# Kernel optimization log

Hardware: AMD Instinct MI355X
Metric: run time of the kernel (lower is better)

## Reference

```python
import jax, jax.numpy as jnp
import numpy as np

B, T, V, F, NH = 2, 1, 4, 128, 9
EMB_ZOOM = 5
N = 12 * 4 ** EMB_ZOOM        # 12288 grid cells at emb_zoom
NUP = 4 * N                   # 49152 cells at zoom emb_zoom+1
NVARS = 8


def setup_inputs() -> dict:
    key = jax.random.key(0)
    ks = jax.random.split(key, 8)
    embeddings = jax.random.normal(ks[0], (NVARS, N, F), dtype=jnp.float32)
    x5 = jax.random.normal(ks[1], (B, T, V, N, F), dtype=jnp.float32)
    x6 = jax.random.normal(ks[2], (B, T, V, NUP, F), dtype=jnp.float32)
    W5 = jax.random.normal(ks[3], (F, 2 * F), dtype=jnp.float32) / np.sqrt(F)
    b5 = jnp.zeros((2 * F,), dtype=jnp.float32)
    W6 = jax.random.normal(ks[4], (NH * F, 8 * F), dtype=jnp.float32) / np.sqrt(NH * F)
    b6 = jnp.zeros((8 * F,), dtype=jnp.float32)
    var_idx = jax.random.randint(ks[5], (B, T, V), 0, NVARS)
    adjc = jax.random.randint(ks[6], (N, NH), 0, N)
    adjc = adjc.at[:, 0].set(jnp.arange(N))  # column 0 is the self index
    return {"embeddings": embeddings, "x5": x5, "x6": x6,
            "W5": W5, "b5": b5, "W6": W6, "b6": b6,
            "var_idx": var_idx, "adjc": adjc}


def reference(embeddings, x5, x6, W5, b5, W6, b6, var_idx, adjc):
    # per-variable embedding selection: (B,T,V,N,F)
    embs = embeddings[var_idx]

    # --- zoom == emb_zoom: gather self index, Linear(F -> 2F), FiLM ---
    e5 = jnp.take(embs, adjc[:, 0], axis=-2)          # (B,T,V,N,F)
    h5 = e5 @ W5 + b5                                  # (B,T,V,N,2F)
    scale5, shift5 = jnp.split(h5, 2, axis=-1)
    y5 = x5 * scale5 + shift5

    # --- zoom == emb_zoom+1: gather full neighborhood, Linear(9F -> 4*2F), FiLM ---
    e6 = jnp.take(embs, adjc.reshape(-1), axis=-2)     # (B,T,V,N*NH,F)
    e6 = e6.reshape(B, T, V, N, NH * F)
    h6 = (e6 @ W6 + b6).reshape(B, T, V, NUP, 2 * F)   # 4 children per coarse cell
    scale6, shift6 = jnp.split(h6, 2, axis=-1)
    y6 = x6 * scale6 + shift6

    return (y5, y6)
```

## Files before the change

kernel.cpp:

```cpp
#include <hip/hip_runtime.h>
#include <stdint.h>

#define F_     128
#define N_     12288
#define NH_    9
#define NSLOT_ 8
#define NVARS_ 8
#define NUP_   (4*N_)
#define K6_    (NH_*F_)

typedef __attribute__((ext_vector_type(8))) short bf16x8;
typedef __attribute__((ext_vector_type(4))) float f32x4;

typedef const __attribute__((address_space(1))) unsigned char* gp1_t;
typedef __attribute__((address_space(3))) unsigned char* lp3_t;

__device__ __forceinline__ void load16(const void* g, void* l) {
  __builtin_amdgcn_global_load_lds((gp1_t)g, (lp3_t)l, 16, 0, 0);
}

__device__ __forceinline__ unsigned short f2bf(float f) {
  union { float f; unsigned int u; } x; x.f = f;
  unsigned int u = x.u;
  unsigned int r = u + 0x7FFFu + ((u >> 16) & 1u);
  return (unsigned short)(r >> 16);
}

__global__ void k_conv_emb(const float4* __restrict__ src, ushort4* __restrict__ dst, int n4) {
  int i = blockIdx.x * blockDim.x + threadIdx.x;
  if (i >= n4) return;
  float4 v = src[i];
  ushort4 o;
  o.x = f2bf(v.x); o.y = f2bf(v.y); o.z = f2bf(v.z); o.w = f2bf(v.w);
  dst[i] = o;
}

__global__ void k_transpose_bf(const float* __restrict__ src, unsigned short* __restrict__ dst,
                               int rows, int cols) {
  int i = blockIdx.x * blockDim.x + threadIdx.x;
  if (i >= rows * cols) return;
  int j = i / rows, k = i % rows;
  dst[i] = f2bf(src[k * cols + j]);
}

__global__ __launch_bounds__(256) void k_h5(
    const unsigned short* __restrict__ embB,
    const unsigned short* __restrict__ W5T,
    const float* __restrict__ b5,
    const float* __restrict__ x5,
    const int* __restrict__ var_idx,
    const int* __restrict__ adjc,
    float* __restrict__ y5)
{
  const int slot = blockIdx.y;
  const int var = var_idx[slot];
  for (int j = 0; j < NSLOT_; ++j) {
    if (j >= slot) break;
    if (var_idx[j] == var) return;
  }
  unsigned int fmask = 0;
  for (int j = slot; j < NSLOT_; ++j)
    if (var_idx[j] == var) fmask |= 1u << j;

  __shared__ __align__(1024) unsigned char smem[8192 + 32768 + 64*4];
  unsigned char* Asm = smem;
  unsigned char* Bsm = smem + 8192;
  int* ald = (int*)(smem + 8192 + 32768);

  const int tid = threadIdx.x;
  const int l = tid & 63, w = tid >> 6;
  const int wr = w >> 1, wc = w & 1;
  const int li8 = l >> 3, pc = l & 7, l15 = l & 15, l16 = l >> 4;

  const int nt = blockIdx.x;
  const int n0 = nt * 64;

  if (tid < 64) ald[tid] = adjc[(n0 + tid) * NH_];
  __syncthreads();

  const f32x4 fz = {0.f, 0.f, 0.f, 0.f};
  f32x4 accS[2][4], accH[2][4];
#pragma unroll
  for (int mf = 0; mf < 2; ++mf)
#pragma unroll
    for (int nf = 0; nf < 4; ++nf) { accS[mf][nf] = fz; accH[mf][nf] = fz; }

  const size_t embVarOff = (size_t)var * ((size_t)N_ * F_);

  for (int step = 0; step < 2; ++step) {
    const int k0 = step << 6;
#pragma unroll
    for (int q2 = 0; q2 < 2; ++q2) {
      const int q = w * 2 + q2;
      const int r = q * 8 + li8;
      const int lc = pc ^ (r & 7);
      const unsigned short* g = embB + embVarOff + (size_t)ald[r] * F_ + k0 + lc * 8;
      load16(g, Asm + q * 1024);
    }
#pragma unroll
    for (int q2 = 0; q2 < 8; ++q2) {
      const int q = w * 8 + q2;
      const int j = q * 8 + li8;
      const int lc = pc ^ (j & 7);
      const unsigned short* g = W5T + (size_t)j * F_ + k0 + lc * 8;
      load16(g, Bsm + q * 1024);
    }
    __syncthreads();

#pragma unroll
    for (int kf = 0; kf < 2; ++kf) {
      const int kc = kf * 4 + l16;
      bf16x8 a[2], bs[4], bh[4];
#pragma unroll
      for (int mf = 0; mf < 2; ++mf) {
        const int r = wr * 32 + mf * 16 + l15;
        a[mf] = *(const bf16x8*)(Asm + r * 128 + ((kc ^ (r & 7)) << 4));
      }
#pragma unroll
      for (int nf = 0; nf < 4; ++nf) {
        const int js = wc * 64 + nf * 16 + l15;
        bs[nf] = *(const bf16x8*)(Bsm + js * 128 + ((kc ^ (js & 7)) << 4));
        const int jh = js + 128;
        bh[nf] = *(const bf16x8*)(Bsm + jh * 128 + ((kc ^ (jh & 7)) << 4));
      }
#pragma unroll
      for (int mf = 0; mf < 2; ++mf)
#pragma unroll
        for (int nf = 0; nf < 4; ++nf) {
          accS[mf][nf] = __builtin_amdgcn_mfma_f32_16x16x32_bf16(a[mf], bs[nf], accS[mf][nf], 0, 0, 0);
          accH[mf][nf] = __builtin_amdgcn_mfma_f32_16x16x32_bf16(a[mf], bh[nf], accH[mf][nf], 0, 0, 0);
        }
    }
    __syncthreads();
  }

  float* SP = (float*)smem;
  float* HP = SP + 32 * 132;
#pragma unroll 1
  for (int mh = 0; mh < 2; ++mh) {
    if (wr == mh) {
#pragma unroll
      for (int mf = 0; mf < 2; ++mf)
#pragma unroll
        for (int nf = 0; nf < 4; ++nf) {
          const int f = wc * 64 + nf * 16 + l15;
          const float sb = b5[f];
          const float hb = b5[128 + f];
#pragma unroll
          for (int reg = 0; reg < 4; ++reg) {
            const int rr = mf * 16 + l16 * 4 + reg;
            SP[rr * 132 + f] = accS[mf][nf][reg] + sb;
            HP[rr * 132 + f] = accH[mf][nf][reg] + hb;
          }
        }
    }
    __syncthreads();
#pragma unroll
    for (int it = 0; it < 4; ++it) {
      const int g = it * 256 + tid;
      const int row = g >> 5, c4 = g & 31;
      const float4 s4 = *(const float4*)(SP + row * 132 + c4 * 4);
      const float4 h4 = *(const float4*)(HP + row * 132 + c4 * 4);
      const size_t nf4 = ((size_t)(n0 + mh * 32 + row)) * F_ + c4 * 4;
      for (int j = slot; j < NSLOT_; ++j) {
        if (!(fmask & (1u << j))) continue;
        const size_t idx = (size_t)j * ((size_t)N_ * F_) + nf4;
        const float4 x = *(const float4*)(x5 + idx);
        float4 y;
        y.x = x.x * s4.x + h4.x;
        y.y = x.y * s4.y + h4.y;
        y.z = x.z * s4.z + h4.z;
        y.w = x.w * s4.w + h4.w;
        *(float4*)(y5 + idx) = y;
      }
    }
    if (mh == 0) __syncthreads();
  }
}

__global__ __launch_bounds__(512) void k_h6(
    const unsigned short* __restrict__ embB,
    const unsigned short* __restrict__ W6T,
    const float* __restrict__ b6,
    const float* __restrict__ x6,
    const int* __restrict__ var_idx,
    const int* __restrict__ adjc,
    float* __restrict__ y6)
{
  const int slot = blockIdx.z;
  const int var = var_idx[slot];
  for (int j = 0; j < NSLOT_; ++j) {
    if (j >= slot) break;
    if (var_idx[j] == var) return;
  }
  unsigned int fmask = 0;
  for (int j = slot; j < NSLOT_; ++j)
    if (var_idx[j] == var) fmask |= 1u << j;

  __shared__ __align__(1024) unsigned char smem[2 * 64 * 132 * 4];
  unsigned char* Asm = smem;
  unsigned char* Bsm = smem + 16384;
  int* ald = (int*)(smem + 16384 + 32768);

  const int tid = threadIdx.x;
  const int l = tid & 63, w = tid >> 6;
  const int wr = w >> 2, wc = w & 3;
  const int li8 = l >> 3, pc = l & 7, l15 = l & 15, l16 = l >> 4;

  const int nt = blockIdx.x;
  const int ct = blockIdx.y;
  const int n0 = nt * 128;
  const int col0 = ct * 256;

  for (int t = tid; t < 128 * NH_; t += 512) ald[t] = adjc[n0 * NH_ + t];
  __syncthreads();

  const f32x4 fz = {0.f, 0.f, 0.f, 0.f};
  f32x4 accS[4][2], accH[4][2];
#pragma unroll
  for (int mf = 0; mf < 4; ++mf)
#pragma unroll
    for (int nf = 0; nf < 2; ++nf) { accS[mf][nf] = fz; accH[mf][nf] = fz; }

  const size_t embVarOff = (size_t)var * ((size_t)N_ * F_);

  for (int step = 0; step < K6_ / 64; ++step) {
    const int h = step >> 1;
    const int kk0 = (step & 1) << 6;
    const int k0 = step << 6;

#pragma unroll
    for (int q2 = 0; q2 < 2; ++q2) {
      const int q = w * 2 + q2;
      const int r = q * 8 + li8;
      const int lc = pc ^ (r & 7);
      const int m = ald[r * NH_ + h];
      const unsigned short* g = embB + embVarOff + (size_t)m * F_ + kk0 + lc * 8;
      load16(g, Asm + q * 1024);
    }
#pragma unroll
    for (int q2 = 0; q2 < 4; ++q2) {
      const int q = w * 4 + q2;
      const int j = q * 8 + li8;
      const int lc = pc ^ (j & 7);
      const unsigned short* g = W6T + (size_t)(col0 + j) * K6_ + k0 + lc * 8;
      load16(g, Bsm + q * 1024);
    }
    __syncthreads();

#pragma unroll
    for (int kf = 0; kf < 2; ++kf) {
      const int kc = kf * 4 + l16;
      bf16x8 a[4], bs[2], bh[2];
#pragma unroll
      for (int mf = 0; mf < 4; ++mf) {
        const int r = wr * 64 + mf * 16 + l15;
        a[mf] = *(const bf16x8*)(Asm + r * 128 + ((kc ^ (r & 7)) << 4));
      }
#pragma unroll
      for (int nf = 0; nf < 2; ++nf) {
        const int js = wc * 32 + nf * 16 + l15;
        bs[nf] = *(const bf16x8*)(Bsm + js * 128 + ((kc ^ (js & 7)) << 4));
        const int jh = js + 128;
        bh[nf] = *(const bf16x8*)(Bsm + jh * 128 + ((kc ^ (jh & 7)) << 4));
      }
#pragma unroll
      for (int mf = 0; mf < 4; ++mf)
#pragma unroll
        for (int nf = 0; nf < 2; ++nf) {
          accS[mf][nf] = __builtin_amdgcn_mfma_f32_16x16x32_bf16(a[mf], bs[nf], accS[mf][nf], 0, 0, 0);
          accH[mf][nf] = __builtin_amdgcn_mfma_f32_16x16x32_bf16(a[mf], bh[nf], accH[mf][nf], 0, 0, 0);
        }
    }
    __syncthreads();
  }

  float* SP = (float*)smem;
  float* HP = SP + 64 * 132;
#pragma unroll 1
  for (int mh = 0; mh < 2; ++mh) {
    if (wr == mh) {
#pragma unroll
      for (int mf = 0; mf < 4; ++mf)
#pragma unroll
        for (int nf = 0; nf < 2; ++nf) {
          const int f = wc * 32 + nf * 16 + l15;
          const float sb = b6[col0 + f];
          const float hb = b6[col0 + 128 + f];
#pragma unroll
          for (int reg = 0; reg < 4; ++reg) {
            const int rr = mf * 16 + l16 * 4 + reg;
            SP[rr * 132 + f] = accS[mf][nf][reg] + sb;
            HP[rr * 132 + f] = accH[mf][nf][reg] + hb;
          }
        }
    }
    __syncthreads();
#pragma unroll
    for (int it = 0; it < 4; ++it) {
      const int g = it * 512 + tid;
      const int row = g >> 5, c4 = g & 31;
      const float4 s4 = *(const float4*)(SP + row * 132 + c4 * 4);
      const float4 h4 = *(const float4*)(HP + row * 132 + c4 * 4);
      const size_t nupf = ((size_t)(4 * (n0 + mh * 64 + row) + ct)) * F_ + c4 * 4;
      for (int j = slot; j < NSLOT_; ++j) {
        if (!(fmask & (1u << j))) continue;
        const size_t idx = (size_t)j * ((size_t)NUP_ * F_) + nupf;
        const float4 x = *(const float4*)(x6 + idx);
        float4 y;
        y.x = x.x * s4.x + h4.x;
        y.y = x.y * s4.y + h4.y;
        y.z = x.z * s4.z + h4.z;
        y.w = x.w * s4.w + h4.w;
        *(float4*)(y6 + idx) = y;
      }
    }
    if (mh == 0) __syncthreads();
  }
}

extern "C" void kernel_launch(void* const* d_in, const int* in_sizes, int n_in,
                              void* d_out, int out_size, void* d_ws, size_t ws_size,
                              hipStream_t stream) {
  (void)in_sizes; (void)n_in; (void)out_size; (void)ws_size;
  const float* emb = (const float*)d_in[0];
  const float* x5  = (const float*)d_in[1];
  const float* x6  = (const float*)d_in[2];
  const float* W5  = (const float*)d_in[3];
  const float* b5  = (const float*)d_in[4];
  const float* W6  = (const float*)d_in[5];
  const float* b6  = (const float*)d_in[6];
  const int* var_idx = (const int*)d_in[7];
  const int* adjc    = (const int*)d_in[8];

  float* y5 = (float*)d_out;
  float* y6 = y5 + (size_t)NSLOT_ * N_ * F_;

  unsigned short* embB = (unsigned short*)d_ws;
  unsigned short* W5T  = embB + (size_t)NVARS_ * N_ * F_;
  unsigned short* W6T  = W5T + 256 * 128;

  const int embN4 = NVARS_ * N_ * F_ / 4;
  k_conv_emb<<<(embN4 + 255) / 256, 256, 0, stream>>>((const float4*)emb, (ushort4*)embB, embN4);
  k_transpose_bf<<<(128 * 256 + 255) / 256, 256, 0, stream>>>(W5, W5T, 128, 256);
  k_transpose_bf<<<(1152 * 1024 + 255) / 256, 256, 0, stream>>>(W6, W6T, 1152, 1024);

  k_h6<<<dim3(N_ / 128, 4, NSLOT_), 512, 0, stream>>>(embB, W6T, b6, x6, var_idx, adjc, y6);
  k_h5<<<dim3(N_ / 64, NSLOT_), 256, 0, stream>>>(embB, W5T, b5, x5, var_idx, adjc, y5);
}
```

Before: 266.4 us.

## Fuse h5 and h6 FiLM kernels into one launch; tile the weight transpose

Merges the zoom-5 GEMM+FiLM work into the zoom-6 kernel as an extra grid slice (blockIdx.y == 4), so both run in one launch and the small h5 blocks fill the tail of the h6 grid. The h5 path is retiled to 128 rows with 512 threads to match the fused block shape. The weight transpose kernel is rewritten to use a 32x33 shared-memory tile, giving coalesced reads and writes instead of strided global reads. Risks: the h5 slice uses larger tiles with fewer blocks, and the fused kernel's register and LDS footprint is sized for h6.

Result: slower. 342.3 us (+28.5%).

```diff
diff --git a/kernel.cpp b/kernel.cpp
--- a/kernel.cpp
+++ b/kernel.cpp
@@ -35,156 +35,36 @@
   dst[i] = o;
 }
 
-__global__ void k_transpose_bf(const float* __restrict__ src, unsigned short* __restrict__ dst,
-                               int rows, int cols) {
-  int i = blockIdx.x * blockDim.x + threadIdx.x;
-  if (i >= rows * cols) return;
-  int j = i / rows, k = i % rows;
-  dst[i] = f2bf(src[k * cols + j]);
-}
-
-__global__ __launch_bounds__(256) void k_h5(
+__global__ __launch_bounds__(256) void k_transpose_bf(
+    const float* __restrict__ src, unsigned short* __restrict__ dst, int rows, int cols) {
+  __shared__ float tile[32][33];
+  const int tx = threadIdx.x & 31, ty = threadIdx.x >> 5;
+  const int c = blockIdx.x * 32 + tx;
+#pragma unroll
+  for (int i = 0; i < 4; ++i) {
+    const int r = blockIdx.y * 32 + ty + i * 8;
+    tile[ty + i * 8][tx] = src[(size_t)r * cols + c];
+  }
+  __syncthreads();
+  const int rr = blockIdx.y * 32 + tx;
+#pragma unroll
+  for (int i = 0; i < 4; ++i) {
+    const int cc = blockIdx.x * 32 + ty + i * 8;
+    dst[(size_t)cc * rows + rr] = f2bf(tile[tx][ty + i * 8]);
+  }
+}
+
+__global__ __launch_bounds__(512) void k_fused(
     const unsigned short* __restrict__ embB,
     const unsigned short* __restrict__ W5T,
+    const unsigned short* __restrict__ W6T,
     const float* __restrict__ b5,
+    const float* __restrict__ b6,
     const float* __restrict__ x5,
-    const int* __restrict__ var_idx,
-    const int* __restrict__ adjc,
-    float* __restrict__ y5)
-{
-  const int slot = blockIdx.y;
-  const int var = var_idx[slot];
-  for (int j = 0; j < NSLOT_; ++j) {
-    if (j >= slot) break;
-    if (var_idx[j] == var) return;
-  }
-  unsigned int fmask = 0;
-  for (int j = slot; j < NSLOT_; ++j)
-    if (var_idx[j] == var) fmask |= 1u << j;
-
-  __shared__ __align__(1024) unsigned char smem[8192 + 32768 + 64*4];
-  unsigned char* Asm = smem;
-  unsigned char* Bsm = smem + 8192;
-  int* ald = (int*)(smem + 8192 + 32768);
-
-  const int tid = threadIdx.x;
-  const int l = tid & 63, w = tid >> 6;
-  const int wr = w >> 1, wc = w & 1;
-  const int li8 = l >> 3, pc = l & 7, l15 = l & 15, l16 = l >> 4;
-
-  const int nt = blockIdx.x;
-  const int n0 = nt * 64;
-
-  if (tid < 64) ald[tid] = adjc[(n0 + tid) * NH_];
-  __syncthreads();
-
-  const f32x4 fz = {0.f, 0.f, 0.f, 0.f};
-  f32x4 accS[2][4], accH[2][4];
-#pragma unroll
-  for (int mf = 0; mf < 2; ++mf)
-#pragma unroll
-    for (int nf = 0; nf < 4; ++nf) { accS[mf][nf] = fz; accH[mf][nf] = fz; }
-
-  const size_t embVarOff = (size_t)var * ((size_t)N_ * F_);
-
-  for (int step = 0; step < 2; ++step) {
-    const int k0 = step << 6;
-#pragma unroll
-    for (int q2 = 0; q2 < 2; ++q2) {
-      const int q = w * 2 + q2;
-      const int r = q * 8 + li8;
-      const int lc = pc ^ (r & 7);
-      const unsigned short* g = embB + embVarOff + (size_t)ald[r] * F_ + k0 + lc * 8;
-      load16(g, Asm + q * 1024);
-    }
-#pragma unroll
-    for (int q2 = 0; q2 < 8; ++q2) {
-      const int q = w * 8 + q2;
-      const int j = q * 8 + li8;
-      const int lc = pc ^ (j & 7);
-      const unsigned short* g = W5T + (size_t)j * F_ + k0 + lc * 8;
-      load16(g, Bsm + q * 1024);
-    }
-    __syncthreads();
-
-#pragma unroll
-    for (int kf = 0; kf < 2; ++kf) {
-      const int kc = kf * 4 + l16;
-      bf16x8 a[2], bs[4], bh[4];
-#pragma unroll
-      for (int mf = 0; mf < 2; ++mf) {
-        const int r = wr * 32 + mf * 16 + l15;
-        a[mf] = *(const bf16x8*)(Asm + r * 128 + ((kc ^ (r & 7)) << 4));
-      }
-#pragma unroll
-      for (int nf = 0; nf < 4; ++nf) {
-        const int js = wc * 64 + nf * 16 + l15;
-        bs[nf] = *(const bf16x8*)(Bsm + js * 128 + ((kc ^ (js & 7)) << 4));
-        const int jh = js + 128;
-        bh[nf] = *(const bf16x8*)(Bsm + jh * 128 + ((kc ^ (jh & 7)) << 4));
-      }
-#pragma unroll
-      for (int mf = 0; mf < 2; ++mf)
-#pragma unroll
-        for (int nf = 0; nf < 4; ++nf) {
-          accS[mf][nf] = __builtin_amdgcn_mfma_f32_16x16x32_bf16(a[mf], bs[nf], accS[mf][nf], 0, 0, 0);
-          accH[mf][nf] = __builtin_amdgcn_mfma_f32_16x16x32_bf16(a[mf], bh[nf], accH[mf][nf], 0, 0, 0);
-        }
-    }
-    __syncthreads();
-  }
-
-  float* SP = (float*)smem;
-  float* HP = SP + 32 * 132;
-#pragma unroll 1
-  for (int mh = 0; mh < 2; ++mh) {
-    if (wr == mh) {
-#pragma unroll
-      for (int mf = 0; mf < 2; ++mf)
-#pragma unroll
-        for (int nf = 0; nf < 4; ++nf) {
-          const int f = wc * 64 + nf * 16 + l15;
-          const float sb = b5[f];
-          const float hb = b5[128 + f];
-#pragma unroll
-          for (int reg = 0; reg < 4; ++reg) {
-            const int rr = mf * 16 + l16 * 4 + reg;
-            SP[rr * 132 + f] = accS[mf][nf][reg] + sb;
-            HP[rr * 132 + f] = accH[mf][nf][reg] + hb;
-          }
-        }
-    }
-    __syncthreads();
-#pragma unroll
-    for (int it = 0; it < 4; ++it) {
-      const int g = it * 256 + tid;
-      const int row = g >> 5, c4 = g & 31;
-      const float4 s4 = *(const float4*)(SP + row * 132 + c4 * 4);
-      const float4 h4 = *(const float4*)(HP + row * 132 + c4 * 4);
-      const size_t nf4 = ((size_t)(n0 + mh * 32 + row)) * F_ + c4 * 4;
-      for (int j = slot; j < NSLOT_; ++j) {
-        if (!(fmask & (1u << j))) continue;
-        const size_t idx = (size_t)j * ((size_t)N_ * F_) + nf4;
-        const float4 x = *(const float4*)(x5 + idx);
-        float4 y;
-        y.x = x.x * s4.x + h4.x;
-        y.y = x.y * s4.y + h4.y;
-        y.z = x.z * s4.z + h4.z;
-        y.w = x.w * s4.w + h4.w;
-        *(float4*)(y5 + idx) = y;
-      }
-    }
-    if (mh == 0) __syncthreads();
-  }
-}
-
-__global__ __launch_bounds__(512) void k_h6(
-    const unsigned short* __restrict__ embB,
-    const unsigned short* __restrict__ W6T,
-    const float* __restrict__ b6,
     const float* __restrict__ x6,
     const int* __restrict__ var_idx,
     const int* __restrict__ adjc,
+    float* __restrict__ y5,
     float* __restrict__ y6)
 {
   const int slot = blockIdx.z;
@@ -208,9 +88,8 @@
   const int li8 = l >> 3, pc = l & 7, l15 = l & 15, l16 = l >> 4;
 
   const int nt = blockIdx.x;
-  const int ct = blockIdx.y;
+  const int cz = blockIdx.y;
   const int n0 = nt * 128;
-  const int col0 = ct * 256;
 
   for (int t = tid; t < 128 * NH_; t += 512) ald[t] = adjc[n0 * NH_ + t];
   __syncthreads();
@@ -223,6 +102,103 @@
     for (int nf = 0; nf < 2; ++nf) { accS[mf][nf] = fz; accH[mf][nf] = fz; }
 
   const size_t embVarOff = (size_t)var * ((size_t)N_ * F_);
+  float* SP = (float*)smem;
+  float* HP = SP + 64 * 132;
+
+  if (cz == 4) {
+    for (int step = 0; step < 2; ++step) {
+      const int k0 = step << 6;
+#pragma unroll
+      for (int q2 = 0; q2 < 2; ++q2) {
+        const int q = w * 2 + q2;
+        const int r = q * 8 + li8;
+        const int lc = pc ^ (r & 7);
+        const int m = ald[r * NH_];
+        const unsigned short* g = embB + embVarOff + (size_t)m * F_ + k0 + lc * 8;
+        load16(g, Asm + q * 1024);
+      }
+#pragma unroll
+      for (int q2 = 0; q2 < 4; ++q2) {
+        const int q = w * 4 + q2;
+        const int j = q * 8 + li8;
+        const int lc = pc ^ (j & 7);
+        const unsigned short* g = W5T + (size_t)j * 128 + k0 + lc * 8;
+        load16(g, Bsm + q * 1024);
+      }
+      __syncthreads();
+
+#pragma unroll
+      for (int kf = 0; kf < 2; ++kf) {
+        const int kc = kf * 4 + l16;
+        bf16x8 a[4], bs[2], bh[2];
+#pragma unroll
+        for (int mf = 0; mf < 4; ++mf) {
+          const int r = wr * 64 + mf * 16 + l15;
+          a[mf] = *(const bf16x8*)(Asm + r * 128 + ((kc ^ (r & 7)) << 4));
+        }
+#pragma unroll
+        for (int nf = 0; nf < 2; ++nf) {
+          const int js = wc * 32 + nf * 16 + l15;
+          bs[nf] = *(const bf16x8*)(Bsm + js * 128 + ((kc ^ (js & 7)) << 4));
+          const int jh = js + 128;
+          bh[nf] = *(const bf16x8*)(Bsm + jh * 128 + ((kc ^ (jh & 7)) << 4));
+        }
+#pragma unroll
+        for (int mf = 0; mf < 4; ++mf)
+#pragma unroll
+          for (int nf = 0; nf < 2; ++nf) {
+            accS[mf][nf] = __builtin_amdgcn_mfma_f32_16x16x32_bf16(a[mf], bs[nf], accS[mf][nf], 0, 0, 0);
+            accH[mf][nf] = __builtin_amdgcn_mfma_f32_16x16x32_bf16(a[mf], bh[nf], accH[mf][nf], 0, 0, 0);
+          }
+      }
+      __syncthreads();
+    }
+
+#pragma unroll 1
+    for (int mh = 0; mh < 2; ++mh) {
+      if (wr == mh) {
+#pragma unroll
+        for (int mf = 0; mf < 4; ++mf)
+#pragma unroll
+          for (int nf = 0; nf < 2; ++nf) {
+            const int f = wc * 32 + nf * 16 + l15;
+            const float sb = b5[f];
+            const float hb = b5[128 + f];
+#pragma unroll
+            for (int reg = 0; reg < 4; ++reg) {
+              const int rr = mf * 16 + l16 * 4 + reg;
+              SP[rr * 132 + f] = accS[mf][nf][reg] + sb;
+              HP[rr * 132 + f] = accH[mf][nf][reg] + hb;
+            }
+          }
+      }
+      __syncthreads();
+#pragma unroll
+      for (int it = 0; it < 4; ++it) {
+        const int g = it * 512 + tid;
+        const int row = g >> 5, c4 = g & 31;
+        const float4 s4 = *(const float4*)(SP + row * 132 + c4 * 4);
+        const float4 h4 = *(const float4*)(HP + row * 132 + c4 * 4);
+        const size_t nf4 = ((size_t)(n0 + mh * 64 + row)) * F_ + c4 * 4;
+        for (int j = slot; j < NSLOT_; ++j) {
+          if (!(fmask & (1u << j))) continue;
+          const size_t idx = (size_t)j * ((size_t)N_ * F_) + nf4;
+          const float4 x = *(const float4*)(x5 + idx);
+          float4 y;
+          y.x = x.x * s4.x + h4.x;
+          y.y = x.y * s4.y + h4.y;
+          y.z = x.z * s4.z + h4.z;
+          y.w = x.w * s4.w + h4.w;
+          *(float4*)(y5 + idx) = y;
+        }
+      }
+      if (mh == 0) __syncthreads();
+    }
+    return;
+  }
+
+  const int ct = cz;
+  const int col0 = ct * 256;
 
   for (int step = 0; step < K6_ / 64; ++step) {
     const int h = step >> 1;
@@ -275,8 +251,6 @@
     __syncthreads();
   }
 
-  float* SP = (float*)smem;
-  float* HP = SP + 64 * 132;
 #pragma unroll 1
   for (int mh = 0; mh < 2; ++mh) {
     if (wr == mh) {
@@ -342,9 +316,9 @@
 
   const int embN4 = NVARS_ * N_ * F_ / 4;
   k_conv_emb<<<(embN4 + 255) / 256, 256, 0, stream>>>((const float4*)emb, (ushort4*)embB, embN4);
-  k_transpose_bf<<<(128 * 256 + 255) / 256, 256, 0, stream>>>(W5, W5T, 128, 256);
-  k_transpose_bf<<<(1152 * 1024 + 255) / 256, 256, 0, stream>>>(W6, W6T, 1152, 1024);
-
-  k_h6<<<dim3(N_ / 128, 4, NSLOT_), 512, 0, stream>>>(embB, W6T, b6, x6, var_idx, adjc, y6);
-  k_h5<<<dim3(N_ / 64, NSLOT_), 256, 0, stream>>>(embB, W5T, b5, x5, var_idx, adjc, y5);
-}
+  k_transpose_bf<<<dim3(256 / 32, 128 / 32), 256, 0, stream>>>(W5, W5T, 128, 256);
+  k_transpose_bf<<<dim3(1024 / 32, 1152 / 32), 256, 0, stream>>>(W6, W6T, 1152, 1024);
+
+  k_fused<<<dim3(N_ / 128, 5, NSLOT_), 512, 0, stream>>>(
+      embB, W5T, W6T, b5, b6, x5, x6, var_idx, adjc, y5, y6);
+}
```

## Split h6 column tiles into halves with 256-thread blocks and tiled weight transpose

Applied to the files above, without the earlier changes.

The h6 GEMM block now covers 64 scale and 64 shift columns instead of 128 each, using 4 waves instead of 8, which doubles the grid along the column dimension and shrinks LDS use so more blocks can be resident per CU. In exchange, each block gathers the embedding A-tile for fewer output columns, so the irregular gather traffic is repeated twice as often. Separately, the weight transpose kernel is rewritten as a 32x32 shared-memory tile transpose so that both the reads and the writes are coalesced.

Result: slower. 332.0 us (+24.6%).

```diff
diff --git a/kernel.cpp b/kernel.cpp
--- a/kernel.cpp
+++ b/kernel.cpp
@@ -35,12 +35,23 @@
   dst[i] = o;
 }
 
-__global__ void k_transpose_bf(const float* __restrict__ src, unsigned short* __restrict__ dst,
-                               int rows, int cols) {
-  int i = blockIdx.x * blockDim.x + threadIdx.x;
-  if (i >= rows * cols) return;
-  int j = i / rows, k = i % rows;
-  dst[i] = f2bf(src[k * cols + j]);
+__global__ __launch_bounds__(256) void k_transpose_bf(
+    const float* __restrict__ src, unsigned short* __restrict__ dst, int rows, int cols) {
+  __shared__ float tile[32][33];
+  const int tx = threadIdx.x & 31, ty = threadIdx.x >> 5;
+  const int c = blockIdx.x * 32 + tx;
+#pragma unroll
+  for (int i = 0; i < 4; ++i) {
+    const int r = blockIdx.y * 32 + ty + i * 8;
+    tile[ty + i * 8][tx] = src[(size_t)r * cols + c];
+  }
+  __syncthreads();
+  const int rr = blockIdx.y * 32 + tx;
+#pragma unroll
+  for (int i = 0; i < 4; ++i) {
+    const int cc = blockIdx.x * 32 + ty + i * 8;
+    dst[(size_t)cc * rows + rr] = f2bf(tile[tx][ty + i * 8]);
+  }
 }
 
 __global__ __launch_bounds__(256) void k_h5(
@@ -178,7 +189,7 @@
   }
 }
 
-__global__ __launch_bounds__(512) void k_h6(
+__global__ __launch_bounds__(256) void k_h6(
     const unsigned short* __restrict__ embB,
     const unsigned short* __restrict__ W6T,
     const float* __restrict__ b6,
@@ -197,22 +208,23 @@
   for (int j = slot; j < NSLOT_; ++j)
     if (var_idx[j] == var) fmask |= 1u << j;
 
-  __shared__ __align__(1024) unsigned char smem[2 * 64 * 132 * 4];
+  __shared__ __align__(1024) unsigned char smem[16384 + 16384 + 128*NH_*4];
   unsigned char* Asm = smem;
   unsigned char* Bsm = smem + 16384;
-  int* ald = (int*)(smem + 16384 + 32768);
+  int* ald = (int*)(smem + 32768);
 
   const int tid = threadIdx.x;
   const int l = tid & 63, w = tid >> 6;
-  const int wr = w >> 2, wc = w & 3;
+  const int wr = w >> 1, wc = w & 1;
   const int li8 = l >> 3, pc = l & 7, l15 = l & 15, l16 = l >> 4;
 
   const int nt = blockIdx.x;
-  const int ct = blockIdx.y;
+  const int ct = blockIdx.y >> 1;
+  const int s  = blockIdx.y & 1;
   const int n0 = nt * 128;
-  const int col0 = ct * 256;
-
-  for (int t = tid; t < 128 * NH_; t += 512) ald[t] = adjc[n0 * NH_ + t];
+  const int cb = ct * 256 + s * 64;
+
+  for (int t = tid; t < 128 * NH_; t += 256) ald[t] = adjc[n0 * NH_ + t];
   __syncthreads();
 
   const f32x4 fz = {0.f, 0.f, 0.f, 0.f};
@@ -230,8 +242,8 @@
     const int k0 = step << 6;
 
 #pragma unroll
-    for (int q2 = 0; q2 < 2; ++q2) {
-      const int q = w * 2 + q2;
+    for (int q2 = 0; q2 < 4; ++q2) {
+      const int q = w * 4 + q2;
       const int r = q * 8 + li8;
       const int lc = pc ^ (r & 7);
       const int m = ald[r * NH_ + h];
@@ -243,7 +255,8 @@
       const int q = w * 4 + q2;
       const int j = q * 8 + li8;
       const int lc = pc ^ (j & 7);
-      const unsigned short* g = W6T + (size_t)(col0 + j) * K6_ + k0 + lc * 8;
+      const int wrow = cb + (j & 63) + ((j >> 6) << 7);
+      const unsigned short* g = W6T + (size_t)wrow * K6_ + k0 + lc * 8;
       load16(g, Bsm + q * 1024);
     }
     __syncthreads();
@@ -261,7 +274,7 @@
       for (int nf = 0; nf < 2; ++nf) {
         const int js = wc * 32 + nf * 16 + l15;
         bs[nf] = *(const bf16x8*)(Bsm + js * 128 + ((kc ^ (js & 7)) << 4));
-        const int jh = js + 128;
+        const int jh = js + 64;
         bh[nf] = *(const bf16x8*)(Bsm + jh * 128 + ((kc ^ (jh & 7)) << 4));
       }
 #pragma unroll
@@ -276,7 +289,7 @@
   }
 
   float* SP = (float*)smem;
-  float* HP = SP + 64 * 132;
+  float* HP = SP + 64 * 68;
 #pragma unroll 1
   for (int mh = 0; mh < 2; ++mh) {
     if (wr == mh) {
@@ -285,24 +298,24 @@
 #pragma unroll
         for (int nf = 0; nf < 2; ++nf) {
           const int f = wc * 32 + nf * 16 + l15;
-          const float sb = b6[col0 + f];
-          const float hb = b6[col0 + 128 + f];
+          const float sb = b6[cb + f];
+          const float hb = b6[cb + 128 + f];
 #pragma unroll
           for (int reg = 0; reg < 4; ++reg) {
             const int rr = mf * 16 + l16 * 4 + reg;
-            SP[rr * 132 + f] = accS[mf][nf][reg] + sb;
-            HP[rr * 132 + f] = accH[mf][nf][reg] + hb;
+            SP[rr * 68 + f] = accS[mf][nf][reg] + sb;
+            HP[rr * 68 + f] = accH[mf][nf][reg] + hb;
           }
         }
     }
     __syncthreads();
 #pragma unroll
     for (int it = 0; it < 4; ++it) {
-      const int g = it * 512 + tid;
-      const int row = g >> 5, c4 = g & 31;
-      const float4 s4 = *(const float4*)(SP + row * 132 + c4 * 4);
-      const float4 h4 = *(const float4*)(HP + row * 132 + c4 * 4);
-      const size_t nupf = ((size_t)(4 * (n0 + mh * 64 + row) + ct)) * F_ + c4 * 4;
+      const int g = it * 256 + tid;
+      const int row = g >> 4, c4 = g & 15;
+      const float4 s4 = *(const float4*)(SP + row * 68 + c4 * 4);
+      const float4 h4 = *(const float4*)(HP + row * 68 + c4 * 4);
+      const size_t nupf = ((size_t)(4 * (n0 + mh * 64 + row) + ct)) * F_ + cb - ct * 256 + c4 * 4;
       for (int j = slot; j < NSLOT_; ++j) {
         if (!(fmask & (1u << j))) continue;
         const size_t idx = (size_t)j * ((size_t)NUP_ * F_) + nupf;
@@ -342,9 +355,9 @@
 
   const int embN4 = NVARS_ * N_ * F_ / 4;
   k_conv_emb<<<(embN4 + 255) / 256, 256, 0, stream>>>((const float4*)emb, (ushort4*)embB, embN4);
-  k_transpose_bf<<<(128 * 256 + 255) / 256, 256, 0, stream>>>(W5, W5T, 128, 256);
-  k_transpose_bf<<<(1152 * 1024 + 255) / 256, 256, 0, stream>>>(W6, W6T, 1152, 1024);
-
-  k_h6<<<dim3(N_ / 128, 4, NSLOT_), 512, 0, stream>>>(embB, W6T, b6, x6, var_idx, adjc, y6);
+  k_transpose_bf<<<dim3(256 / 32, 128 / 32), 256, 0, stream>>>(W5, W5T, 128, 256);
+  k_transpose_bf<<<dim3(1024 / 32, 1152 / 32), 256, 0, stream>>>(W6, W6T, 1152, 1024);
+
+  k_h6<<<dim3(N_ / 128, 8, NSLOT_), 256, 0, stream>>>(embB, W6T, b6, x6, var_idx, adjc, y6);
   k_h5<<<dim3(N_ / 64, NSLOT_), 256, 0, stream>>>(embB, W5T, b5, x5, var_idx, adjc, y5);
 }
```
